# Kernel optimization log

Hardware: AMD Instinct MI355X
Metric: run time of the kernel (lower is better)

Reference implementation:

```python
import jax, jax.numpy as jnp
import numpy as np

B, S, H = 8, 4096, 1024
N_IDX = 65536
N_SEG = 8192


def setup_inputs() -> dict:
    key = jax.random.key(0)
    k1, k2, k3, k4, k5 = jax.random.split(key, 5)
    transformer_hidden = jax.random.normal(k1, (B, S, H), dtype=jnp.float32)
    indices = jax.random.randint(k2, (N_IDX,), 0, B * S, dtype=jnp.int32)
    segment_ids = jnp.sort(jax.random.randint(k3, (N_IDX,), 0, N_SEG, dtype=jnp.int32))
    W_dense = jax.random.normal(k4, (H, H), dtype=jnp.float32) * (1.0 / np.sqrt(H))
    b_dense = jnp.zeros((H,), dtype=jnp.float32)
    W_proj = jax.random.normal(k5, (1, H), dtype=jnp.float32) * (1.0 / np.sqrt(H))
    b_proj = jnp.zeros((1,), dtype=jnp.float32)
    return {
        "transformer_hidden": transformer_hidden,
        "indices": indices,
        "segment_ids": segment_ids,
        "W_dense": W_dense,
        "b_dense": b_dense,
        "W_proj": W_proj,
        "b_proj": b_proj,
    }


def reference(transformer_hidden, indices, segment_ids, W_dense, b_dense, W_proj, b_proj):
    # Flatten tokens: [B*S, H]
    hid = transformer_hidden.reshape(-1, transformer_hidden.shape[-1])
    # Ragged gather of grouped token indices, then per-group mean (segment mean)
    gathered = hid[indices]  # [n_idx, H]
    sums = jax.ops.segment_sum(gathered, segment_ids, num_segments=N_SEG)  # [G, H]
    counts = jax.ops.segment_sum(
        jnp.ones((indices.shape[0],), dtype=hid.dtype), segment_ids, num_segments=N_SEG
    )
    h = sums / jnp.maximum(counts, 1.0)[:, None]  # [G, H] group means
    # dense -> gelu (torch exact erf gelu) -> lin_proj -> flatten
    z = jax.nn.gelu(h @ W_dense.T + b_dense, approximate=False)
    predictions = z @ W_proj.T + b_proj  # [G, 1]
    return predictions.reshape(-1)
```

## Files before the change

### kernel.cpp

```cpp
#include <hip/hip_runtime.h>
#include <stdint.h>

#define BH   (8 * 4096)
#define HDIM 1024
#define NIDX 65536
#define NSEG 8192
#define KD   1024
#define ND   1024

typedef __bf16 bf16x8 __attribute__((ext_vector_type(8)));
typedef float  f32x4  __attribute__((ext_vector_type(4)));

__device__ __forceinline__ unsigned short f2bf(float f) {
  unsigned int u = __float_as_uint(f);
  u += 0x7fffu + ((u >> 16) & 1u);
  return (unsigned short)(u >> 16);
}

__device__ __forceinline__ void async16(const void* g, void* l) {
  __builtin_amdgcn_global_load_lds(
      (const __attribute__((address_space(1))) void*)g,
      (__attribute__((address_space(3))) void*)l,
      16, 0, 0);
}

__global__ void prep_kernel(const float* __restrict__ W, unsigned short* __restrict__ Wb,
                            const int* __restrict__ seg, int* __restrict__ starts) {
  if (blockIdx.x < 1024) {
    int i = (blockIdx.x * 256 + threadIdx.x) * 4;
    float4 v = *(const float4*)(W + i);
    ushort4 o;
    o.x = f2bf(v.x); o.y = f2bf(v.y); o.z = f2bf(v.z); o.w = f2bf(v.w);
    *(ushort4*)(Wb + i) = o;
  } else {
    int i = (blockIdx.x - 1024) * 256 + threadIdx.x;
    if (i > NIDX) return;
    int prev = (i == 0) ? -1 : seg[i - 1];
    int cur  = (i == NIDX) ? NSEG : seg[i];
    for (int g = prev + 1; g <= cur; ++g) starts[g] = i;
  }
}

__global__ void segmean_kernel(const float* __restrict__ hid,
                               const int* __restrict__ indices,
                               const int* __restrict__ starts,
                               unsigned short* __restrict__ hb,
                               float* __restrict__ out,
                               const float* __restrict__ b_proj) {
  const int g = blockIdx.x;
  const int t = threadIdx.x;
  const int start = starts[g];
  const int end   = starts[g + 1];
  const int col   = t * 4;

  float4 a0 = make_float4(0.f, 0.f, 0.f, 0.f);
  float4 a1 = a0, a2 = a0, a3 = a0;

  int i = start;
  for (; i + 4 <= end; i += 4) {
    int r0 = indices[i];
    int r1 = indices[i + 1];
    int r2 = indices[i + 2];
    int r3 = indices[i + 3];
    float4 v0 = *(const float4*)(hid + (size_t)r0 * HDIM + col);
    float4 v1 = *(const float4*)(hid + (size_t)r1 * HDIM + col);
    float4 v2 = *(const float4*)(hid + (size_t)r2 * HDIM + col);
    float4 v3 = *(const float4*)(hid + (size_t)r3 * HDIM + col);
    a0.x += v0.x; a0.y += v0.y; a0.z += v0.z; a0.w += v0.w;
    a1.x += v1.x; a1.y += v1.y; a1.z += v1.z; a1.w += v1.w;
    a2.x += v2.x; a2.y += v2.y; a2.z += v2.z; a2.w += v2.w;
    a3.x += v3.x; a3.y += v3.y; a3.z += v3.z; a3.w += v3.w;
  }
  for (; i < end; ++i) {
    int r = indices[i];
    float4 v = *(const float4*)(hid + (size_t)r * HDIM + col);
    a0.x += v.x; a0.y += v.y; a0.z += v.z; a0.w += v.w;
  }
  a0.x += a1.x + a2.x + a3.x;
  a0.y += a1.y + a2.y + a3.y;
  a0.z += a1.z + a2.z + a3.z;
  a0.w += a1.w + a2.w + a3.w;

  const float inv = 1.0f / fmaxf((float)(end - start), 1.0f);
  ushort4 o;
  o.x = f2bf(a0.x * inv); o.y = f2bf(a0.y * inv);
  o.z = f2bf(a0.z * inv); o.w = f2bf(a0.w * inv);
  *(ushort4*)(hb + (size_t)g * HDIM + col) = o;

  if (t == 0) out[g] = b_proj[0];
}

__global__ void __launch_bounds__(512)
gemm_gelu_proj_kernel(const unsigned short* __restrict__ A,
                      const unsigned short* __restrict__ Bw,
                      const float* __restrict__ b_dense,
                      const float* __restrict__ w_proj,
                      float* __restrict__ out) {
  __shared__ alignas(16) unsigned short As[128 * 64];
  __shared__ alignas(16) unsigned short Bs[128 * 64];

  const int tid  = threadIdx.x;
  const int lane = tid & 63;
  const int wave = tid >> 6;
  const int wm   = wave >> 2;
  const int wn   = wave & 3;
  const int m0   = blockIdx.x * 128;
  const int n0   = blockIdx.y * 128;
  const int lr   = lane & 15;
  const int quad = lane >> 4;

  f32x4 acc[4][2];
#pragma unroll
  for (int mi = 0; mi < 4; ++mi)
#pragma unroll
    for (int ni = 0; ni < 2; ++ni) {
      acc[mi][ni][0] = 0.f; acc[mi][ni][1] = 0.f;
      acc[mi][ni][2] = 0.f; acc[mi][ni][3] = 0.f;
    }

  for (int kt = 0; kt < KD / 64; ++kt) {
    const int k0 = kt * 64;
#pragma unroll
    for (int j = 0; j < 2; ++j) {
      int c   = j * 512 + wave * 64 + lane;
      int row = c >> 3, sl = c & 7;
      int kcg = sl ^ (row & 7);
      async16(A + (size_t)(m0 + row) * KD + k0 + kcg * 8,
              (char*)As + (j * 512 + wave * 64) * 16);
    }
#pragma unroll
    for (int j = 0; j < 2; ++j) {
      int c   = j * 512 + wave * 64 + lane;
      int row = c >> 3, sl = c & 7;
      int kcg = sl ^ (row & 7);
      async16(Bw + (size_t)(n0 + row) * KD + k0 + kcg * 8,
              (char*)Bs + (j * 512 + wave * 64) * 16);
    }
    __syncthreads();

#pragma unroll
    for (int s = 0; s < 2; ++s) {
      bf16x8 af[4], bf_[2];
#pragma unroll
      for (int i = 0; i < 4; ++i) {
        int ra   = wm * 64 + i * 16 + lr;
        int slot = (s * 4 + quad) ^ (ra & 7);
        af[i] = *(const bf16x8*)(As + ra * 64 + slot * 8);
      }
#pragma unroll
      for (int i = 0; i < 2; ++i) {
        int rb   = wn * 32 + i * 16 + lr;
        int slot = (s * 4 + quad) ^ (rb & 7);
        bf_[i] = *(const bf16x8*)(Bs + rb * 64 + slot * 8);
      }
#pragma unroll
      for (int mi = 0; mi < 4; ++mi)
#pragma unroll
        for (int ni = 0; ni < 2; ++ni)
          acc[mi][ni] = __builtin_amdgcn_mfma_f32_16x16x32_bf16(af[mi], bf_[ni], acc[mi][ni], 0, 0, 0);
    }
    __syncthreads();
  }

#pragma unroll
  for (int mi = 0; mi < 4; ++mi) {
    float rp[4] = {0.f, 0.f, 0.f, 0.f};
#pragma unroll
    for (int ni = 0; ni < 2; ++ni) {
      int col  = n0 + wn * 32 + ni * 16 + lr;
      float bd = b_dense[col];
      float wp = w_proj[col];
#pragma unroll
      for (int r = 0; r < 4; ++r) {
        float v  = acc[mi][ni][r] + bd;
        float gl = 0.5f * v * (1.0f + erff(v * 0.70710678118654752f));
        rp[r] += gl * wp;
      }
    }
#pragma unroll
    for (int r = 0; r < 4; ++r) {
      float c = rp[r];
      c += __shfl_xor(c, 1);
      c += __shfl_xor(c, 2);
      c += __shfl_xor(c, 4);
      c += __shfl_xor(c, 8);
      if (lr == 0)
        atomicAdd(out + (m0 + wm * 64 + mi * 16 + quad * 4 + r), c);
    }
  }
}

extern "C" void kernel_launch(void* const* d_in, const int* in_sizes, int n_in,
                              void* d_out, int out_size, void* d_ws, size_t ws_size,
                              hipStream_t stream) {
  const float* hid     = (const float*)d_in[0];
  const int*   indices = (const int*)d_in[1];
  const int*   seg     = (const int*)d_in[2];
  const float* W_dense = (const float*)d_in[3];
  const float* b_dense = (const float*)d_in[4];
  const float* W_proj  = (const float*)d_in[5];
  const float* b_proj  = (const float*)d_in[6];
  float* out = (float*)d_out;

  unsigned short* hb     = (unsigned short*)d_ws;
  unsigned short* Wb     = (unsigned short*)((char*)d_ws + (size_t)NSEG * KD * 2);
  int*            starts = (int*)((char*)d_ws + (size_t)NSEG * KD * 2 + (size_t)ND * KD * 2);

  prep_kernel<<<dim3(1024 + (NIDX + 256) / 256), 256, 0, stream>>>(W_dense, Wb, seg, starts);
  segmean_kernel<<<dim3(NSEG), 256, 0, stream>>>(hid, indices, starts, hb, out, b_proj);
  gemm_gelu_proj_kernel<<<dim3(NSEG / 128, ND / 128), 512, 0, stream>>>(hb, Wb, b_dense, W_proj, out);
}
```

Measured before the change: 234.8 us.

## Double-buffer LDS tiles in the GEMM-GELU-projection kernel

The A and B shared-memory tiles become two buffers. The first K-tile is loaded before the loop, and each iteration issues the async global-to-LDS loads for the next tile before running the MFMAs on the current one. This removes the barrier between load and compute in each iteration, so memory latency can overlap with matrix math. In exchange, LDS use per block doubles to 64KB, which can lower occupancy. The end-of-iteration barrier is what makes the prefetched data visible.

```diff
diff --git a/kernel.cpp b/kernel.cpp
--- a/kernel.cpp
+++ b/kernel.cpp
@@ -96,8 +96,8 @@
                       const float* __restrict__ b_dense,
                       const float* __restrict__ w_proj,
                       float* __restrict__ out) {
-  __shared__ alignas(16) unsigned short As[128 * 64];
-  __shared__ alignas(16) unsigned short Bs[128 * 64];
+  __shared__ alignas(16) unsigned short As[2][128 * 64];
+  __shared__ alignas(16) unsigned short Bs[2][128 * 64];
 
   const int tid  = threadIdx.x;
   const int lane = tid & 63;
@@ -118,25 +118,43 @@
       acc[mi][ni][2] = 0.f; acc[mi][ni][3] = 0.f;
     }
 
+#pragma unroll
+  for (int j = 0; j < 2; ++j) {
+    int c = j * 512 + tid;
+    int row = c >> 3, sl = c & 7;
+    int kcg = sl ^ (row & 7);
+    async16(A + (size_t)(m0 + row) * KD + kcg * 8, (char*)As[0] + (size_t)c * 16);
+  }
+#pragma unroll
+  for (int j = 0; j < 2; ++j) {
+    int c = j * 512 + tid;
+    int row = c >> 3, sl = c & 7;
+    int kcg = sl ^ (row & 7);
+    async16(Bw + (size_t)(n0 + row) * KD + kcg * 8, (char*)Bs[0] + (size_t)c * 16);
+  }
+  __syncthreads();
+
   for (int kt = 0; kt < KD / 64; ++kt) {
-    const int k0 = kt * 64;
-#pragma unroll
-    for (int j = 0; j < 2; ++j) {
-      int c   = j * 512 + wave * 64 + lane;
-      int row = c >> 3, sl = c & 7;
-      int kcg = sl ^ (row & 7);
-      async16(A + (size_t)(m0 + row) * KD + k0 + kcg * 8,
-              (char*)As + (j * 512 + wave * 64) * 16);
-    }
-#pragma unroll
-    for (int j = 0; j < 2; ++j) {
-      int c   = j * 512 + wave * 64 + lane;
-      int row = c >> 3, sl = c & 7;
-      int kcg = sl ^ (row & 7);
-      async16(Bw + (size_t)(n0 + row) * KD + k0 + kcg * 8,
-              (char*)Bs + (j * 512 + wave * 64) * 16);
-    }
-    __syncthreads();
+    const int cur = kt & 1;
+    if (kt + 1 < KD / 64) {
+      const int k0n = (kt + 1) * 64;
+#pragma unroll
+      for (int j = 0; j < 2; ++j) {
+        int c = j * 512 + tid;
+        int row = c >> 3, sl = c & 7;
+        int kcg = sl ^ (row & 7);
+        async16(A + (size_t)(m0 + row) * KD + k0n + kcg * 8,
+                (char*)As[cur ^ 1] + (size_t)c * 16);
+      }
+#pragma unroll
+      for (int j = 0; j < 2; ++j) {
+        int c = j * 512 + tid;
+        int row = c >> 3, sl = c & 7;
+        int kcg = sl ^ (row & 7);
+        async16(Bw + (size_t)(n0 + row) * KD + k0n + kcg * 8,
+                (char*)Bs[cur ^ 1] + (size_t)c * 16);
+      }
+    }
 
 #pragma unroll
     for (int s = 0; s < 2; ++s) {
@@ -145,13 +163,13 @@
       for (int i = 0; i < 4; ++i) {
         int ra   = wm * 64 + i * 16 + lr;
         int slot = (s * 4 + quad) ^ (ra & 7);
-        af[i] = *(const bf16x8*)(As + ra * 64 + slot * 8);
+        af[i] = *(const bf16x8*)(As[cur] + ra * 64 + slot * 8);
       }
 #pragma unroll
       for (int i = 0; i < 2; ++i) {
         int rb   = wn * 32 + i * 16 + lr;
         int slot = (s * 4 + quad) ^ (rb & 7);
-        bf_[i] = *(const bf16x8*)(Bs + rb * 64 + slot * 8);
+        bf_[i] = *(const bf16x8*)(Bs[cur] + rb * 64 + slot * 8);
       }
 #pragma unroll
       for (int mi = 0; mi < 4; ++mi)
```

New measurement: 236.2 us. No clear change (+0.6%).
